# Kernel tuning notes

Hardware: AMD Instinct MI355X
Metric: run time of the kernel (lower is better)

## Reference

```python
import math
import jax, jax.numpy as jnp
import numpy as np

B, S, D, H = 2, 2048, 1024, 16
Dh = D // H
EPS = 1e-5


def layernorm(x, g, b):
    mu = jnp.mean(x, axis=-1, keepdims=True)
    var = jnp.mean(jnp.square(x - mu), axis=-1, keepdims=True)
    return (x - mu) * jax.lax.rsqrt(var + EPS) * g + b


def setup_inputs() -> dict:
    key = jax.random.key(0)
    ks = jax.random.split(key, 8)
    sc = 0.02
    return {
        "x": jax.random.normal(ks[0], (B, S, D), jnp.float32),
        # per-head wq weights stacked: [H, D, Dh] (wk/wv are unused in the original)
        "wq_w": jax.random.normal(ks[1], (H, D, Dh), jnp.float32) * sc,
        "wq_b": jnp.zeros((H, Dh), jnp.float32),
        "fc_w": jax.random.normal(ks[2], (D, D), jnp.float32) * sc,
        "fc_b": jnp.zeros((D,), jnp.float32),
        "ln1_g": jnp.ones((D,), jnp.float32),
        "ln1_b": jnp.zeros((D,), jnp.float32),
        "w1": jax.random.normal(ks[3], (D, 4 * D), jnp.float32) * sc,
        "b1": jnp.zeros((4 * D,), jnp.float32),
        "w2": jax.random.normal(ks[4], (4 * D, D), jnp.float32) * sc,
        "b2": jnp.zeros((D,), jnp.float32),
        "ln2_g": jnp.ones((D,), jnp.float32),
        "ln2_b": jnp.zeros((D,), jnp.float32),
    }


def reference(x, wq_w, wq_b, fc_w, fc_b, ln1_g, ln1_b, w1, b1, w2, b2, ln2_g, ln2_b):
    # NOTE: original bug — wq is applied to q, k and v; since q=k=v=x, Q=K=V.
    qh = jnp.einsum("bsd,hde->bhse", x, wq_w) + wq_b[None, :, None, :]  # [B,H,S,Dh]
    scores = jnp.einsum("bhse,bhte->bhst", qh, qh) / math.sqrt(Dh)      # [B,H,S,S]
    attn = jax.nn.softmax(scores, axis=-1)
    ctx = jnp.einsum("bhst,bhte->bhse", attn, qh)                        # [B,H,S,Dh]
    # concat heads along last dim (head h -> columns h*Dh:(h+1)*Dh)
    y = jnp.transpose(ctx, (0, 2, 1, 3)).reshape(B, S, D)
    y = y @ fc_w + fc_b
    y = layernorm(y + x, ln1_g, ln1_b)
    y1 = jax.nn.relu(y @ w1 + b1) @ w2 + b2
    return layernorm(y + y1, ln2_g, ln2_b)
```

## Files before the change

### kernel.cpp

```cpp
#include <hip/hip_runtime.h>
#include <hip/hip_bf16.h>

typedef unsigned short u16;
typedef __bf16 bf16x8 __attribute__((ext_vector_type(8)));
typedef float floatx4 __attribute__((ext_vector_type(4)));

__device__ __forceinline__ float bf2f_u(u16 u) {
    union { unsigned int i; float f; } x; x.i = ((unsigned int)u) << 16; return x.f;
}
__device__ __forceinline__ u16 f2bf_u(float f) {
    union { float f; unsigned int i; } x; x.f = f;
    unsigned int r = x.i + 0x7fffu + ((x.i >> 16) & 1u);
    return (u16)(r >> 16);
}

__device__ __forceinline__ void gl_lds16(const void* g, void* l) {
    __builtin_amdgcn_global_load_lds(
        (const __attribute__((address_space(1))) void*)g,
        (__attribute__((address_space(3))) void*)l, 16, 0, 0);
}

__global__ __launch_bounds__(256) void tobf_k(const float* __restrict__ in,
                                              u16* __restrict__ out) {
    int i = (blockIdx.x * 256 + threadIdx.x) * 8;
    float4 v0 = *(const float4*)&in[i];
    float4 v1 = *(const float4*)&in[i + 4];
    u16 tmp[8] = {f2bf_u(v0.x), f2bf_u(v0.y), f2bf_u(v0.z), f2bf_u(v0.w),
                  f2bf_u(v1.x), f2bf_u(v1.y), f2bf_u(v1.z), f2bf_u(v1.w)};
    *(uint4*)&out[i] = *(const uint4*)tmp;
}

__global__ __launch_bounds__(256) void transpose_bf_k(
    const float* __restrict__ in, u16* __restrict__ out,
    int R, int C, size_t inZ, size_t outZ)
{
    __shared__ u16 T[64][80];
    const float* ip = in + blockIdx.z * inZ;
    u16* op = out + blockIdx.z * outZ;
    const int r0 = blockIdx.y * 64, c0 = blockIdx.x * 64;
    const int t = threadIdx.x;
#pragma unroll
    for (int i = 0; i < 4; i++) {
        int c = t + i * 256;
        int rr = c >> 4, cc = (c & 15) * 4;
        float4 v = *(const float4*)&ip[(size_t)(r0 + rr) * C + c0 + cc];
        T[cc + 0][rr] = f2bf_u(v.x); T[cc + 1][rr] = f2bf_u(v.y);
        T[cc + 2][rr] = f2bf_u(v.z); T[cc + 3][rr] = f2bf_u(v.w);
    }
    __syncthreads();
#pragma unroll
    for (int i = 0; i < 2; i++) {
        int c = t + i * 256;
        int oc = c >> 3, k8 = (c & 7) * 8;
        uint4 v = *(const uint4*)&T[oc][k8];
        *(uint4*)&op[(size_t)(c0 + oc) * R + r0 + k8] = v;
    }
}

__global__ __launch_bounds__(256) void gemm_bt64_k(
    const u16* __restrict__ A, const u16* __restrict__ Bt,
    int gm, int gn, int N, int K, int ldb,
    const float* __restrict__ bias, const u16* __restrict__ resid,
    float* __restrict__ out, u16* __restrict__ out_bf, int mode)
{
    __shared__ __align__(16) u16 As[2][128 * 64];
    __shared__ __align__(16) u16 Bs[2][64 * 64];

    const int id = blockIdx.x;
    const int xcd = id & 7, s = id >> 3;
    const int bandM = gm >> 2, bandN = gn >> 1;
    const int m0 = ((xcd >> 1) * bandM + (s % bandM)) * 128;
    const int n0 = ((xcd & 1) * bandN + (s / bandM)) * 64;

    const int t = threadIdx.x;
    const int wid = t >> 6, lane = t & 63;
    const int wm = (wid >> 1) * 64, wn = (wid & 1) * 32;
    const int lr = lane & 15, quad = lane >> 4;
    const int srow = lane >> 3;
    const int scol = ((lane & 7) ^ (lane >> 3)) * 8;

    floatx4 acc[4][2];
#pragma unroll
    for (int i = 0; i < 4; i++)
#pragma unroll
        for (int j = 0; j < 2; j++)
            acc[i][j] = (floatx4){0.f, 0.f, 0.f, 0.f};

    auto stage = [&](int b, int k0) {
#pragma unroll
        for (int i = 0; i < 4; i++) {
            int rb = wid * 32 + i * 8;
            gl_lds16(&A[(size_t)(m0 + rb + srow) * K + k0 + scol], &As[b][rb * 64]);
        }
#pragma unroll
        for (int i = 0; i < 2; i++) {
            int rb = wid * 16 + i * 8;
            gl_lds16(&Bt[(size_t)(n0 + rb + srow) * ldb + k0 + scol], &Bs[b][rb * 64]);
        }
    };

    stage(0, 0);
    __syncthreads();

    int cur = 0;
    for (int k0 = 0; k0 < K; k0 += 64) {
        if (k0 + 64 < K) stage(cur ^ 1, k0 + 64);

#pragma unroll
        for (int kk = 0; kk < 2; kk++) {
            bf16x8 af[4], bfr[2];
#pragma unroll
            for (int i = 0; i < 4; i++) {
                int R = wm + i * 16 + lr;
                int c = ((kk * 4 + quad) ^ (lr & 7)) * 8;
                af[i] = *(const bf16x8*)&As[cur][R * 64 + c];
            }
#pragma unroll
            for (int j = 0; j < 2; j++) {
                int R = wn + j * 16 + lr;
                int c = ((kk * 4 + quad) ^ (lr & 7)) * 8;
                bfr[j] = *(const bf16x8*)&Bs[cur][R * 64 + c];
            }
#pragma unroll
            for (int i = 0; i < 4; i++)
#pragma unroll
                for (int j = 0; j < 2; j++)
                    acc[i][j] = __builtin_amdgcn_mfma_f32_16x16x32_bf16(af[i], bfr[j], acc[i][j], 0, 0, 0);
        }

        __syncthreads();
        cur ^= 1;
    }

#pragma unroll
    for (int i = 0; i < 4; i++) {
#pragma unroll
        for (int j = 0; j < 2; j++) {
#pragma unroll
            for (int r = 0; r < 4; r++) {
                int grow = m0 + wm + i * 16 + quad * 4 + r;
                int gcol = n0 + wn + j * 16 + lr;
                float val = acc[i][j][r];
                if (bias) val += bias[gcol];
                if (mode == 0) {
                    int bb = grow >> 11, ss = grow & 2047;
                    int h = gcol >> 6, e = gcol & 63;
                    out_bf[(((size_t)bb * 16 + h) * 2048 + ss) * 64 + e] = f2bf_u(val);
                } else if (mode == 1) {
                    size_t idx = (size_t)grow * N + gcol;
                    out[idx] = val + bf2f_u(resid[idx]);
                } else if (mode == 2) {
                    out_bf[(size_t)grow * N + gcol] = f2bf_u(fmaxf(val, 0.f));
                } else if (mode == 3) {
                    size_t idx = (size_t)grow * N + gcol;
                    out[idx] = out[idx] + val;
                } else {
                    size_t idx = (size_t)grow * N + gcol;
                    out_bf[idx] = f2bf_u(val + bf2f_u(resid[idx]));
                }
            }
        }
    }
}

#define KST 72
#define PST 68
__global__ __launch_bounds__(256) void attn_mfma_k(const u16* __restrict__ qh,
                                                   u16* __restrict__ ctx)
{
    __shared__ __align__(16) u16 Ks[64][KST];
    __shared__ __align__(16) u16 Vt[64][KST];
    __shared__ __align__(16) u16 Ps[4][2][16][PST];

    const int bh = blockIdx.x >> 4;
    const int qb = blockIdx.x & 15;
    const u16* __restrict__ base = qh + (size_t)bh * (2048 * 64);
    const int t = threadIdx.x, wid = t >> 6, lane = t & 63;
    const int lr = lane & 15, quad = lane >> 4;
    const int q0 = qb * 128 + wid * 16;

    bf16x8 af[2][2];
#pragma unroll
    for (int f = 0; f < 2; f++) {
        af[f][0] = *(const bf16x8*)&base[(size_t)(q0 + f * 64 + lr) * 64 + quad * 8];
        af[f][1] = *(const bf16x8*)&base[(size_t)(q0 + f * 64 + lr) * 64 + quad * 8 + 32];
    }

    floatx4 Of[2][4];
#pragma unroll
    for (int f = 0; f < 2; f++)
#pragma unroll
        for (int dt = 0; dt < 4; dt++) Of[f][dt] = (floatx4){0.f, 0.f, 0.f, 0.f};
    float lsum[2] = {0.f, 0.f};

    const int src0 = t >> 3;
    const int src1 = (t + 256) >> 3;
    const int scol = (t & 7) * 8;

    uint4 stg[2];
    stg[0] = *(const uint4*)&base[(size_t)src0 * 64 + scol];
    stg[1] = *(const uint4*)&base[(size_t)src1 * 64 + scol];
    {
#pragma unroll
        for (int cc = 0; cc < 2; cc++) {
            int row = cc ? src1 : src0;
            *(uint4*)&Ks[row][scol] = stg[cc];
            const u16* pv = (const u16*)&stg[cc];
#pragma unroll
            for (int i = 0; i < 8; i++) {
                int d = scol + i;
                Vt[d][row ^ (d & 0x38)] = pv[i];
            }
        }
    }

    for (int kt = 0; kt < 2048; kt += 64) {
        __syncthreads();
        const bool pf = (kt + 64) < 2048;
        if (pf) {
            stg[0] = *(const uint4*)&base[(size_t)(kt + 64 + src0) * 64 + scol];
            stg[1] = *(const uint4*)&base[(size_t)(kt + 64 + src1) * 64 + scol];
        }

#pragma unroll
        for (int nt = 0; nt < 4; nt++) {
            bf16x8 b0 = *(const bf16x8*)&Ks[nt * 16 + lr][quad * 8];
            bf16x8 b1 = *(const bf16x8*)&Ks[nt * 16 + lr][quad * 8 + 32];
#pragma unroll
            for (int f = 0; f < 2; f++) {
                floatx4 z = (floatx4){0.f, 0.f, 0.f, 0.f};
                z = __builtin_amdgcn_mfma_f32_16x16x32_bf16(b0, af[f][0], z, 0, 0, 0);
                z = __builtin_amdgcn_mfma_f32_16x16x32_bf16(b1, af[f][1], z, 0, 0, 0);
                float p0 = __expf(fminf(z[0] * 0.125f, 60.f));
                float p1 = __expf(fminf(z[1] * 0.125f, 60.f));
                float p2 = __expf(fminf(z[2] * 0.125f, 60.f));
                float p3 = __expf(fminf(z[3] * 0.125f, 60.f));
                lsum[f] += (p0 + p1) + (p2 + p3);
                unsigned int lo, hi;
                asm("v_cvt_pk_bf16_f32 %0, %1, %2" : "=v"(lo) : "v"(p0), "v"(p1));
                asm("v_cvt_pk_bf16_f32 %0, %1, %2" : "=v"(hi) : "v"(p2), "v"(p3));
                uint2 pk; pk.x = lo; pk.y = hi;
                *(uint2*)&Ps[wid][f][lr][nt * 16 + quad * 4] = pk;
            }
        }

        bf16x8 aP[2][2];
#pragma unroll
        for (int f = 0; f < 2; f++) {
            aP[f][0] = *(const bf16x8*)&Ps[wid][f][lr][quad * 8];
            aP[f][1] = *(const bf16x8*)&Ps[wid][f][lr][quad * 8 + 32];
        }
        __builtin_amdgcn_s_setprio(1);
#pragma unroll
        for (int dt = 0; dt < 4; dt++) {
            int d = dt * 16 + lr, msk = d & 0x38;
            bf16x8 b0 = *(const bf16x8*)&Vt[d][(quad * 8) ^ msk];
            bf16x8 b1 = *(const bf16x8*)&Vt[d][(32 + quad * 8) ^ msk];
#pragma unroll
            for (int f = 0; f < 2; f++) {
                Of[f][dt] = __builtin_amdgcn_mfma_f32_16x16x32_bf16(aP[f][0], b0, Of[f][dt], 0, 0, 0);
                Of[f][dt] = __builtin_amdgcn_mfma_f32_16x16x32_bf16(aP[f][1], b1, Of[f][dt], 0, 0, 0);
            }
        }
        __builtin_amdgcn_s_setprio(0);

        __syncthreads();
        if (pf) {
#pragma unroll
            for (int cc = 0; cc < 2; cc++) {
                int row = cc ? src1 : src0;
                *(uint4*)&Ks[row][scol] = stg[cc];
                const u16* pv = (const u16*)&stg[cc];
#pragma unroll
                for (int i = 0; i < 8; i++) {
                    int d = scol + i;
                    Vt[d][row ^ (d & 0x38)] = pv[i];
                }
            }
        }
    }

    const int b = bh >> 4, h = bh & 15;
#pragma unroll
    for (int f = 0; f < 2; f++) {
        float l = lsum[f];
        l += __shfl_xor(l, 16);
        l += __shfl_xor(l, 32);
#pragma unroll
        for (int r = 0; r < 4; r++) {
            float lq = __shfl(l, quad * 4 + r);
            float inv = 1.f / lq;
            size_t rowoff = ((size_t)b * 2048 + q0 + f * 64 + quad * 4 + r) * 1024 + h * 64;
#pragma unroll
            for (int dt = 0; dt < 4; dt++)
                ctx[rowoff + dt * 16 + lr] = f2bf_u(Of[f][dt][r] * inv);
        }
    }
}

__global__ __launch_bounds__(256) void ln_k(const void* __restrict__ in,
                                            const float* __restrict__ g,
                                            const float* __restrict__ b,
                                            float* __restrict__ out_f,
                                            u16* __restrict__ out_bf, int icode)
{
    const int row = blockIdx.x;
    const int t = threadIdx.x;
    float4 v;
    if (icode) {
        v = *(const float4*)&((const float*)in)[(size_t)row * 1024 + t * 4];
    } else {
        ushort4 u = *(const ushort4*)&((const u16*)in)[(size_t)row * 1024 + t * 4];
        v.x = bf2f_u(u.x); v.y = bf2f_u(u.y); v.z = bf2f_u(u.z); v.w = bf2f_u(u.w);
    }
    float s  = v.x + v.y + v.z + v.w;
    float ss = v.x * v.x + v.y * v.y + v.z * v.z + v.w * v.w;
#pragma unroll
    for (int off = 32; off >= 1; off >>= 1) {
        s  += __shfl_down(s, off);
        ss += __shfl_down(ss, off);
    }
    __shared__ float sm[10];
    const int wid = t >> 6, lane = t & 63;
    if (lane == 0) { sm[wid] = s; sm[4 + wid] = ss; }
    __syncthreads();
    if (t == 0) {
        float S  = sm[0] + sm[1] + sm[2] + sm[3];
        float SS = sm[4] + sm[5] + sm[6] + sm[7];
        float mu = S * (1.f / 1024.f);
        float var = SS * (1.f / 1024.f) - mu * mu;
        sm[8] = mu; sm[9] = rsqrtf(fmaxf(var, 0.f) + 1e-5f);
    }
    __syncthreads();
    float mu = sm[8], rs = sm[9];
    float4 G  = *(const float4*)&g[t * 4];
    float4 Bv = *(const float4*)&b[t * 4];
    float r0 = (v.x - mu) * rs * G.x + Bv.x;
    float r1 = (v.y - mu) * rs * G.y + Bv.y;
    float r2 = (v.z - mu) * rs * G.z + Bv.z;
    float r3 = (v.w - mu) * rs * G.w + Bv.w;
    if (out_f) {
        float4 ov = {r0, r1, r2, r3};
        *(float4*)&out_f[(size_t)row * 1024 + t * 4] = ov;
    }
    if (out_bf) {
        ushort4 ou = {f2bf_u(r0), f2bf_u(r1), f2bf_u(r2), f2bf_u(r3)};
        *(ushort4*)&out_bf[(size_t)row * 1024 + t * 4] = ou;
    }
}

extern "C" void kernel_launch(void* const* d_in, const int* in_sizes, int n_in,
                              void* d_out, int out_size, void* d_ws, size_t ws_size,
                              hipStream_t stream)
{
    const float* x    = (const float*)d_in[0];
    const float* wq_w = (const float*)d_in[1];
    const float* wq_b = (const float*)d_in[2];
    const float* fc_w = (const float*)d_in[3];
    const float* fc_b = (const float*)d_in[4];
    const float* ln1g = (const float*)d_in[5];
    const float* ln1b = (const float*)d_in[6];
    const float* w1   = (const float*)d_in[7];
    const float* b1   = (const float*)d_in[8];
    const float* w2   = (const float*)d_in[9];
    const float* b2   = (const float*)d_in[10];
    const float* ln2g = (const float*)d_in[11];
    const float* ln2b = (const float*)d_in[12];

    char* ws = (char*)d_ws;
    const size_t MB = 1024 * 1024;
    u16*   w1_bt  = (u16*)(ws);
    u16*   w2_bt  = (u16*)(ws + 8 * MB);
    u16*   wqm_bt = (u16*)(ws + 16 * MB);
    u16*   fcw_bt = (u16*)(ws + 18 * MB);
    u16*   x_bf   = (u16*)(ws + 20 * MB);
    u16*   qh     = (u16*)(ws + 28 * MB);
    u16*   yln1   = (u16*)(ws + 28 * MB);
    u16*   ctx    = (u16*)(ws + 36 * MB);
    u16*   yfc_bf = (u16*)(ws + 44 * MB);
    u16*   h1     = (u16*)(ws + 36 * MB);
    float* z      = (float*)d_out;
    const bool fullN = ws_size >= 69 * MB;

    transpose_bf_k<<<dim3(64, 16), 256, 0, stream>>>(w1, w1_bt, 1024, 4096, 0, 0);
    transpose_bf_k<<<dim3(16, 64), 256, 0, stream>>>(w2, w2_bt, 4096, 1024, 0, 0);
    transpose_bf_k<<<dim3(1, 16, 16), 256, 0, stream>>>(wq_w, wqm_bt, 1024, 64,
                                                        (size_t)1024 * 64, (size_t)64 * 1024);
    transpose_bf_k<<<dim3(16, 16), 256, 0, stream>>>(fc_w, fcw_bt, 1024, 1024, 0, 0);
    tobf_k<<<2048, 256, 0, stream>>>(x, x_bf);

    gemm_bt64_k<<<512, 256, 0, stream>>>(x_bf, wqm_bt, 32, 16, 1024, 1024, 1024,
                                         wq_b, nullptr, nullptr, qh, 0);
    attn_mfma_k<<<512, 256, 0, stream>>>(qh, ctx);
    gemm_bt64_k<<<512, 256, 0, stream>>>(ctx, fcw_bt, 32, 16, 1024, 1024, 1024,
                                         fc_b, x_bf, nullptr, yfc_bf, 4);
    ln_k<<<4096, 256, 0, stream>>>(yfc_bf, ln1g, ln1b, nullptr, yln1, 0);

    if (fullN) {
        gemm_bt64_k<<<2048, 256, 0, stream>>>(yln1, w1_bt, 32, 64, 4096, 1024, 1024,
                                              b1, nullptr, nullptr, h1, 2);
        gemm_bt64_k<<<512, 256, 0, stream>>>(h1, w2_bt, 32, 16, 1024, 4096, 4096,
                                             b2, yln1, z, nullptr, 1);
    } else {
        gemm_bt64_k<<<1024, 256, 0, stream>>>(yln1, w1_bt, 32, 32, 2048, 1024, 1024,
                                              b1, nullptr, nullptr, h1, 2);
        gemm_bt64_k<<<512, 256, 0, stream>>>(h1, w2_bt, 32, 16, 1024, 2048, 4096,
                                             b2, yln1, z, nullptr, 1);
        gemm_bt64_k<<<1024, 256, 0, stream>>>(yln1, w1_bt + (size_t)2048 * 1024, 32, 32,
                                              2048, 1024, 1024,
                                              b1 + 2048, nullptr, nullptr, h1, 2);
        gemm_bt64_k<<<512, 256, 0, stream>>>(h1, w2_bt + 2048, 32, 16, 1024, 2048, 4096,
                                             nullptr, nullptr, z, nullptr, 3);
    }
    ln_k<<<4096, 256, 0, stream>>>(z, ln2g, ln2b, (float*)d_out, nullptr, 1);
}
```

Before: 394.4 us.

## Pre-transpose Q/V and stream K/V tiles into LDS via async double buffering

A new kernel writes a transposed copy of the per-head Q projection, so the attention kernel can load V-transposed tiles directly. The attention kernel now fills double-buffered, XOR-swizzled LDS tiles for K and V with global_load_lds, replacing the register-staged loads and scalar transposing LDS stores. This removes the per-element transpose scatter and the register round trip, and overlaps the next tile's fetch with compute. The cost is one extra kernel launch, an extra global pass over qh, and twice the LDS used for K/V.

```diff
diff --git a/kernel.cpp b/kernel.cpp
--- a/kernel.cpp
+++ b/kernel.cpp
@@ -54,6 +54,34 @@
         int oc = c >> 3, k8 = (c & 7) * 8;
         uint4 v = *(const uint4*)&T[oc][k8];
         *(uint4*)&op[(size_t)(c0 + oc) * R + r0 + k8] = v;
+    }
+}
+
+__global__ __launch_bounds__(256) void transpose_qh_k(const u16* __restrict__ in,
+                                                      u16* __restrict__ out)
+{
+    __shared__ u16 T[64][72];
+    const int bh = blockIdx.y;
+    const int s0 = blockIdx.x * 64;
+    const u16* ip = in + (size_t)bh * (2048 * 64);
+    u16* op = out + (size_t)bh * (64 * 2048);
+    const int t = threadIdx.x;
+#pragma unroll
+    for (int i = 0; i < 2; i++) {
+        int c = t + i * 256;
+        int r = c >> 3, cc = (c & 7) * 8;
+        uint4 v = *(const uint4*)&ip[(size_t)(s0 + r) * 64 + cc];
+        const u16* pv = (const u16*)&v;
+#pragma unroll
+        for (int k = 0; k < 8; k++) T[cc + k][r] = pv[k];
+    }
+    __syncthreads();
+#pragma unroll
+    for (int i = 0; i < 2; i++) {
+        int c = t + i * 256;
+        int d = c >> 3, cs = (c & 7) * 8;
+        uint4 v = *(const uint4*)&T[d][cs];
+        *(uint4*)&op[(size_t)d * 2048 + s0 + cs] = v;
     }
 }
 
@@ -163,18 +191,19 @@
     }
 }
 
-#define KST 72
 #define PST 68
 __global__ __launch_bounds__(256) void attn_mfma_k(const u16* __restrict__ qh,
+                                                   const u16* __restrict__ qhT,
                                                    u16* __restrict__ ctx)
 {
-    __shared__ __align__(16) u16 Ks[64][KST];
-    __shared__ __align__(16) u16 Vt[64][KST];
+    __shared__ __align__(16) u16 Ks[2][64 * 64];
+    __shared__ __align__(16) u16 Vt[2][64 * 64];
     __shared__ __align__(16) u16 Ps[4][2][16][PST];
 
     const int bh = blockIdx.x >> 4;
     const int qb = blockIdx.x & 15;
-    const u16* __restrict__ base = qh + (size_t)bh * (2048 * 64);
+    const u16* __restrict__ base  = qh  + (size_t)bh * (2048 * 64);
+    const u16* __restrict__ baseT = qhT + (size_t)bh * (64 * 2048);
     const int t = threadIdx.x, wid = t >> 6, lane = t & 63;
     const int lr = lane & 15, quad = lane >> 4;
     const int q0 = qb * 128 + wid * 16;
@@ -193,39 +222,32 @@
         for (int dt = 0; dt < 4; dt++) Of[f][dt] = (floatx4){0.f, 0.f, 0.f, 0.f};
     float lsum[2] = {0.f, 0.f};
 
-    const int src0 = t >> 3;
-    const int src1 = (t + 256) >> 3;
-    const int scol = (t & 7) * 8;
-
-    uint4 stg[2];
-    stg[0] = *(const uint4*)&base[(size_t)src0 * 64 + scol];
-    stg[1] = *(const uint4*)&base[(size_t)src1 * 64 + scol];
-    {
-#pragma unroll
-        for (int cc = 0; cc < 2; cc++) {
-            int row = cc ? src1 : src0;
-            *(uint4*)&Ks[row][scol] = stg[cc];
-            const u16* pv = (const u16*)&stg[cc];
-#pragma unroll
-            for (int i = 0; i < 8; i++) {
-                int d = scol + i;
-                Vt[d][row ^ (d & 0x38)] = pv[i];
-            }
-        }
-    }
-
+    const int srow = lane >> 3;
+    const int schk = (lane & 7) ^ srow;
+
+    auto stage = [&](int b, int kt) {
+#pragma unroll
+        for (int i = 0; i < 2; i++) {
+            int rb = (wid * 2 + i) * 8;
+            gl_lds16(&base[(size_t)(kt + rb + srow) * 64 + schk * 8],
+                     &Ks[b][rb * 64]);
+            gl_lds16(&baseT[(size_t)(rb + srow) * 2048 + kt + schk * 8],
+                     &Vt[b][rb * 64]);
+        }
+    };
+
+    stage(0, 0);
+    __syncthreads();
+
+    int buf = 0;
     for (int kt = 0; kt < 2048; kt += 64) {
-        __syncthreads();
-        const bool pf = (kt + 64) < 2048;
-        if (pf) {
-            stg[0] = *(const uint4*)&base[(size_t)(kt + 64 + src0) * 64 + scol];
-            stg[1] = *(const uint4*)&base[(size_t)(kt + 64 + src1) * 64 + scol];
-        }
+        if (kt + 64 < 2048) stage(buf ^ 1, kt + 64);
 
 #pragma unroll
         for (int nt = 0; nt < 4; nt++) {
-            bf16x8 b0 = *(const bf16x8*)&Ks[nt * 16 + lr][quad * 8];
-            bf16x8 b1 = *(const bf16x8*)&Ks[nt * 16 + lr][quad * 8 + 32];
+            int row = nt * 16 + lr, rsw = row & 7;
+            bf16x8 b0 = *(const bf16x8*)&Ks[buf][row * 64 + ((quad ^ rsw) * 8)];
+            bf16x8 b1 = *(const bf16x8*)&Ks[buf][row * 64 + (((quad + 4) ^ rsw) * 8)];
 #pragma unroll
             for (int f = 0; f < 2; f++) {
                 floatx4 z = (floatx4){0.f, 0.f, 0.f, 0.f};
@@ -253,9 +275,9 @@
         __builtin_amdgcn_s_setprio(1);
 #pragma unroll
         for (int dt = 0; dt < 4; dt++) {
-            int d = dt * 16 + lr, msk = d & 0x38;
-            bf16x8 b0 = *(const bf16x8*)&Vt[d][(quad * 8) ^ msk];
-            bf16x8 b1 = *(const bf16x8*)&Vt[d][(32 + quad * 8) ^ msk];
+            int d = dt * 16 + lr, dsw = d & 7;
+            bf16x8 b0 = *(const bf16x8*)&Vt[buf][d * 64 + ((quad ^ dsw) * 8)];
+            bf16x8 b1 = *(const bf16x8*)&Vt[buf][d * 64 + (((quad + 4) ^ dsw) * 8)];
 #pragma unroll
             for (int f = 0; f < 2; f++) {
                 Of[f][dt] = __builtin_amdgcn_mfma_f32_16x16x32_bf16(aP[f][0], b0, Of[f][dt], 0, 0, 0);
@@ -265,19 +287,7 @@
         __builtin_amdgcn_s_setprio(0);
 
         __syncthreads();
-        if (pf) {
-#pragma unroll
-            for (int cc = 0; cc < 2; cc++) {
-                int row = cc ? src1 : src0;
-                *(uint4*)&Ks[row][scol] = stg[cc];
-                const u16* pv = (const u16*)&stg[cc];
-#pragma unroll
-                for (int i = 0; i < 8; i++) {
-                    int d = scol + i;
-                    Vt[d][row ^ (d & 0x38)] = pv[i];
-                }
-            }
-        }
+        buf ^= 1;
     }
 
     const int b = bh >> 4, h = bh & 15;
@@ -378,6 +388,7 @@
     u16*   yln1   = (u16*)(ws + 28 * MB);
     u16*   ctx    = (u16*)(ws + 36 * MB);
     u16*   yfc_bf = (u16*)(ws + 44 * MB);
+    u16*   qhT    = (u16*)(ws + 44 * MB);
     u16*   h1     = (u16*)(ws + 36 * MB);
     float* z      = (float*)d_out;
     const bool fullN = ws_size >= 69 * MB;
@@ -391,7 +402,8 @@
 
     gemm_bt64_k<<<512, 256, 0, stream>>>(x_bf, wqm_bt, 32, 16, 1024, 1024, 1024,
                                          wq_b, nullptr, nullptr, qh, 0);
-    attn_mfma_k<<<512, 256, 0, stream>>>(qh, ctx);
+    transpose_qh_k<<<dim3(32, 32), 256, 0, stream>>>(qh, qhT);
+    attn_mfma_k<<<512, 256, 0, stream>>>(qh, qhT, ctx);
     gemm_bt64_k<<<512, 256, 0, stream>>>(ctx, fcw_bt, 32, 16, 1024, 1024, 1024,
                                          fc_b, x_bf, nullptr, yfc_bf, 4);
     ln_k<<<4096, 256, 0, stream>>>(yfc_bf, ln1g, ln1b, nullptr, yln1, 0);
```

Result: no change. 394.0 us (-0.1%).
